# Optimization experiments

Hardware: AMD Instinct MI355X
Metric: run time of the kernel (lower is better)

The kernel has to match this reference:

```python
import jax, jax.numpy as jnp
import numpy as np

B, H, N, DK, DV = 2, 8, 2048, 64, 64

def setup_inputs() -> dict:
    key = jax.random.key(0)
    k1, k2, k3, k4 = jax.random.split(key, 4)
    q = jax.random.normal(k1, (B, H, N, DK), dtype=jnp.float32)
    k = jax.random.normal(k2, (B, H, N, DK), dtype=jnp.float32)
    v = jax.random.normal(k3, (B, H, N, DV), dtype=jnp.float32)
    # decay mask, strictly positive in (0,1)
    omask = jax.random.uniform(k4, (B, H, N, N), dtype=jnp.float32, minval=1e-3, maxval=1.0)
    return {"q": q, "k": k, "v": v, "omask": omask}

def reference(q, k, v, omask):
    # coefficients from the decay mask
    q_bar_coef = omask[..., :, 0] / jnp.sqrt(omask.sum(axis=-1))  # (B,H,n)
    k_bar_coef = 1.0 / omask[..., :, 0]                            # (B,H,n)
    q_bar = q_bar_coef[..., None] * q                               # (B,H,n,dk)
    k_bar = k_bar_coef[..., None] * k                               # (B,H,n,dk)
    # normalizer P (detached in original)
    T = jnp.cumsum(k_bar, axis=-2)                                  # (B,H,n,dk)
    P = jnp.einsum('bhia,bhia->bhi', T, q_bar)                      # (B,H,n)
    P = jnp.maximum(jnp.abs(jax.lax.stop_gradient(P)), 1.0)[..., None]
    # cumulative outer-product state D: (B,H,n,dk,dv)
    D = jnp.cumsum(jnp.einsum('bhia,bhic->bhiac', k_bar, v), axis=-3)
    O = jnp.einsum('bhia,bhiac->bhic', q_bar, D) / P                # (B,H,n,dv)
    return O
```

## Files before the change

kernel.cpp:

```cpp
#include <hip/hip_runtime.h>
#include <cmath>

constexpr int B_ = 2, H_ = 8, N_ = 2048, DK_ = 64, DV_ = 64;
constexpr int BH_ = B_ * H_;
constexpr int C_ = 64;
constexpr int NC_ = N_ / C_;
constexpr int NCH_ = BH_ * NC_;

__global__ __launch_bounds__(256) void coef_kernel(const float* __restrict__ om,
                                                   float* __restrict__ qc,
                                                   float* __restrict__ kc) {
  int row = blockIdx.x * 4 + (threadIdx.x >> 6);
  int lane = threadIdx.x & 63;
  const float* r = om + (size_t)row * N_;
  float s = 0.f;
#pragma unroll
  for (int kk = 0; kk < N_ / 256; ++kk) {
    float4 v4 = *(const float4*)(r + kk * 256 + lane * 4);
    s += (v4.x + v4.y) + (v4.z + v4.w);
  }
#pragma unroll
  for (int off = 32; off > 0; off >>= 1) s += __shfl_xor(s, off, 64);
  if (lane == 0) {
    float o0 = r[0];
    qc[row] = o0 / sqrtf(s);
    kc[row] = 1.0f / o0;
  }
}

__global__ __launch_bounds__(256) void chunksum_kernel(const float* __restrict__ kg,
                                                       const float* __restrict__ vg,
                                                       const float* __restrict__ kc,
                                                       float* __restrict__ ksum,
                                                       float* __restrict__ kvsum) {
  __shared__ float kb[C_][DK_];
  __shared__ float vs[C_][DV_];
  int chunk = blockIdx.x;
  int bh = chunk / NC_, ci = chunk - bh * NC_;
  int r0 = ci * C_;
  size_t gbase = ((size_t)bh * N_ + r0) * DK_;
  int t = threadIdx.x;
#pragma unroll
  for (int p = 0; p < 4; ++p) {
    int f = t + p * 256;
    int row = f >> 4, col = (f & 15) * 4;
    float sc = kc[bh * N_ + r0 + row];
    float4 k4 = *(const float4*)(kg + gbase + (size_t)f * 4);
    k4.x *= sc; k4.y *= sc; k4.z *= sc; k4.w *= sc;
    *(float4*)&kb[row][col] = k4;
    *(float4*)&vs[row][col] = *(const float4*)(vg + gbase + (size_t)f * 4);
  }
  __syncthreads();
  int dk0 = (t & 15) * 4, dv0 = (t >> 4) * 4;
  float acc[4][4] = {};
  float ks[4] = {};
  for (int r = 0; r < C_; ++r) {
    float4 k4 = *(const float4*)&kb[r][dk0];
    float4 v4 = *(const float4*)&vs[r][dv0];
    float ka[4] = {k4.x, k4.y, k4.z, k4.w};
    float va[4] = {v4.x, v4.y, v4.z, v4.w};
#pragma unroll
    for (int i = 0; i < 4; ++i) {
      ks[i] += ka[i];
#pragma unroll
      for (int j = 0; j < 4; ++j) acc[i][j] += ka[i] * va[j];
    }
  }
  float* kvc = kvsum + (size_t)chunk * (DK_ * DV_);
#pragma unroll
  for (int i = 0; i < 4; ++i) {
    float4 w = make_float4(acc[i][0], acc[i][1], acc[i][2], acc[i][3]);
    *(float4*)(kvc + (size_t)(dk0 + i) * DV_ + dv0) = w;
  }
  if (t < 16) {
#pragma unroll
    for (int i = 0; i < 4; ++i) ksum[(size_t)chunk * DK_ + dk0 + i] = ks[i];
  }
}

__global__ __launch_bounds__(256) void scan_kernel(float* __restrict__ ksum,
                                                   float* __restrict__ kvsum) {
  constexpr int PER = DK_ * DV_ + DK_;
  int idx = blockIdx.x * 256 + threadIdx.x;
  if (idx >= BH_ * PER) return;
  int bh = idx / PER, e = idx - bh * PER;
  float run = 0.f;
  if (e < DK_ * DV_) {
    float* p = kvsum + (size_t)bh * NC_ * (DK_ * DV_) + e;
    for (int ci = 0; ci < NC_; ++ci) {
      float tv = p[(size_t)ci * (DK_ * DV_)];
      p[(size_t)ci * (DK_ * DV_)] = run;
      run += tv;
    }
  } else {
    float* p = ksum + (size_t)bh * NC_ * DK_ + (e - DK_ * DV_);
    for (int ci = 0; ci < NC_; ++ci) {
      float tv = p[(size_t)ci * DK_];
      p[(size_t)ci * DK_] = run;
      run += tv;
    }
  }
}

__global__ __launch_bounds__(256) void out_kernel(const float* __restrict__ qg,
                                                  const float* __restrict__ kg,
                                                  const float* __restrict__ vg,
                                                  const float* __restrict__ qc,
                                                  const float* __restrict__ kc,
                                                  const float* __restrict__ ksum,
                                                  const float* __restrict__ kvsum,
                                                  float* __restrict__ outg) {
  __shared__ float qbT[DK_][C_];
  __shared__ float kbT[DK_][C_];
  __shared__ float vs[C_][DV_];
  int chunk = blockIdx.x;
  int bh = chunk / NC_, ci = chunk - bh * NC_;
  int r0 = ci * C_;
  size_t gbase = ((size_t)bh * N_ + r0) * DK_;
  int t = threadIdx.x;
  {
    int i = t & 63;
    int apart = t >> 6;
    float qsc = qc[bh * N_ + r0 + i];
    float ksc = kc[bh * N_ + r0 + i];
#pragma unroll
    for (int u = 0; u < 4; ++u) {
      int a0 = apart * 16 + u * 4;
      float4 q4 = *(const float4*)(qg + gbase + (size_t)i * DK_ + a0);
      float4 k4 = *(const float4*)(kg + gbase + (size_t)i * DK_ + a0);
      qbT[a0 + 0][i] = q4.x * qsc; qbT[a0 + 1][i] = q4.y * qsc;
      qbT[a0 + 2][i] = q4.z * qsc; qbT[a0 + 3][i] = q4.w * qsc;
      kbT[a0 + 0][i] = k4.x * ksc; kbT[a0 + 1][i] = k4.y * ksc;
      kbT[a0 + 2][i] = k4.z * ksc; kbT[a0 + 3][i] = k4.w * ksc;
    }
#pragma unroll
    for (int p = 0; p < 4; ++p) {
      int f = t + p * 256;
      int row = f >> 4, col = (f & 15) * 4;
      *(float4*)&vs[row][col] = *(const float4*)(vg + gbase + (size_t)f * 4);
    }
  }
  __syncthreads();

  int i0 = (t & 15) * 4, j0 = (t >> 4) * 4;
  float acc[4][4] = {};
  for (int a = 0; a < DK_; ++a) {
    float4 q4 = *(const float4*)&qbT[a][i0];
    float4 k4 = *(const float4*)&kbT[a][j0];
    float qa[4] = {q4.x, q4.y, q4.z, q4.w};
    float kk[4] = {k4.x, k4.y, k4.z, k4.w};
#pragma unroll
    for (int ii = 0; ii < 4; ++ii)
#pragma unroll
      for (int jj = 0; jj < 4; ++jj) acc[ii][jj] += qa[ii] * kk[jj];
  }
  __syncthreads();
  float (*St)[C_] = kbT;
#pragma unroll
  for (int jj = 0; jj < 4; ++jj) {
    int j = j0 + jj;
    float4 w;
    w.x = (j <= i0 + 0) ? acc[0][jj] : 0.f;
    w.y = (j <= i0 + 1) ? acc[1][jj] : 0.f;
    w.z = (j <= i0 + 2) ? acc[2][jj] : 0.f;
    w.w = (j <= i0 + 3) ? acc[3][jj] : 0.f;
    *(float4*)&St[j][i0] = w;
  }
  __syncthreads();

  {
    int bi0 = (t >> 4) * 4, c0 = (t & 15) * 4;
    const float* kvp = kvsum + (size_t)chunk * (DK_ * DV_);
    const float* tp = ksum + (size_t)chunk * DK_;
    float o[4][4] = {};
    float pp[4] = {};
    for (int a = 0; a < DK_; ++a) {
      float4 q4 = *(const float4*)&qbT[a][bi0];
      float4 d4 = *(const float4*)(kvp + (size_t)a * DV_ + c0);
      float tv = tp[a];
      float qa[4] = {q4.x, q4.y, q4.z, q4.w};
      float da[4] = {d4.x, d4.y, d4.z, d4.w};
#pragma unroll
      for (int ii = 0; ii < 4; ++ii) {
        pp[ii] += qa[ii] * tv;
#pragma unroll
        for (int cc = 0; cc < 4; ++cc) o[ii][cc] += qa[ii] * da[cc];
      }
    }
    for (int j = 0; j < C_; ++j) {
      float4 s4 = *(const float4*)&St[j][bi0];
      float4 v4 = *(const float4*)&vs[j][c0];
      float sa[4] = {s4.x, s4.y, s4.z, s4.w};
      float va[4] = {v4.x, v4.y, v4.z, v4.w};
#pragma unroll
      for (int ii = 0; ii < 4; ++ii) {
        pp[ii] += sa[ii];
#pragma unroll
        for (int cc = 0; cc < 4; ++cc) o[ii][cc] += sa[ii] * va[cc];
      }
    }
    float* ob = outg + ((size_t)bh * N_ + r0) * DV_;
#pragma unroll
    for (int ii = 0; ii < 4; ++ii) {
      float P = fmaxf(fabsf(pp[ii]), 1.0f);
      float inv = 1.0f / P;
      float4 w = make_float4(o[ii][0] * inv, o[ii][1] * inv,
                             o[ii][2] * inv, o[ii][3] * inv);
      *(float4*)(ob + (size_t)(bi0 + ii) * DV_ + c0) = w;
    }
  }
}

extern "C" void kernel_launch(void* const* d_in, const int* in_sizes, int n_in,
                              void* d_out, int out_size, void* d_ws, size_t ws_size,
                              hipStream_t stream) {
  const float* q = (const float*)d_in[0];
  const float* k = (const float*)d_in[1];
  const float* v = (const float*)d_in[2];
  const float* om = (const float*)d_in[3];
  float* out = (float*)d_out;

  float* ws = (float*)d_ws;
  float* qc = ws;
  float* kc = qc + BH_ * N_;
  float* ksum = kc + BH_ * N_;
  float* kv = ksum + (size_t)NCH_ * DK_;

  coef_kernel<<<BH_ * N_ / 4, 256, 0, stream>>>(om, qc, kc);
  chunksum_kernel<<<NCH_, 256, 0, stream>>>(k, v, kc, ksum, kv);
  constexpr int SCAN_TOTAL = BH_ * (DK_ * DV_ + DK_);
  scan_kernel<<<(SCAN_TOTAL + 255) / 256, 256, 0, stream>>>(ksum, kv);
  out_kernel<<<NCH_, 256, 0, stream>>>(q, k, v, qc, kc, ksum, kv, out);
}
```

Before: 77.06 us.

## Fuse coefficient, chunk-sum, scan and output into one cooperative kernel

Replaces the four-kernel pipeline with a single cooperative kernel of 512 blocks that uses grid-wide syncs between the chunk-sum, scan and output phases. Each block computes the omask row-sum coefficients for its own 64 rows, keeps q/k/v in registers across the phases, and writes the scan to separate buffers so it no longer works in place. This removes three kernel launches and the round trips of the coefficient arrays through global memory. In exchange it adds two grid barriers, needs all 512 blocks resident at once (launch_bounds 256,2), and runs the scan on only a fraction of the threads while the other blocks wait.

Result: slower. 193.0 us (+150.5%).

```diff
diff --git a/kernel.cpp b/kernel.cpp
--- a/kernel.cpp
+++ b/kernel.cpp
@@ -1,5 +1,8 @@
 #include <hip/hip_runtime.h>
+#include <hip/hip_cooperative_groups.h>
 #include <cmath>
+
+namespace cg = cooperative_groups;
 
 constexpr int B_ = 2, H_ = 8, N_ = 2048, DK_ = 64, DV_ = 64;
 constexpr int BH_ = B_ * H_;
@@ -7,138 +10,138 @@
 constexpr int NC_ = N_ / C_;
 constexpr int NCH_ = BH_ * NC_;
 
-__global__ __launch_bounds__(256) void coef_kernel(const float* __restrict__ om,
-                                                   float* __restrict__ qc,
-                                                   float* __restrict__ kc) {
-  int row = blockIdx.x * 4 + (threadIdx.x >> 6);
-  int lane = threadIdx.x & 63;
-  const float* r = om + (size_t)row * N_;
-  float s = 0.f;
-#pragma unroll
-  for (int kk = 0; kk < N_ / 256; ++kk) {
-    float4 v4 = *(const float4*)(r + kk * 256 + lane * 4);
-    s += (v4.x + v4.y) + (v4.z + v4.w);
-  }
-#pragma unroll
-  for (int off = 32; off > 0; off >>= 1) s += __shfl_xor(s, off, 64);
-  if (lane == 0) {
-    float o0 = r[0];
-    qc[row] = o0 / sqrtf(s);
-    kc[row] = 1.0f / o0;
-  }
-}
-
-__global__ __launch_bounds__(256) void chunksum_kernel(const float* __restrict__ kg,
-                                                       const float* __restrict__ vg,
-                                                       const float* __restrict__ kc,
-                                                       float* __restrict__ ksum,
-                                                       float* __restrict__ kvsum) {
+__global__ __launch_bounds__(256, 2) void fused_kernel(
+    const float* __restrict__ qg, const float* __restrict__ kg,
+    const float* __restrict__ vg, const float* __restrict__ om,
+    float* __restrict__ lksum, float* __restrict__ lkv,
+    float* __restrict__ pksum, float* __restrict__ pkv,
+    float* __restrict__ outg)
+{
   __shared__ float kb[C_][DK_];
+  __shared__ float kbT[DK_][C_];
   __shared__ float vs[C_][DV_];
-  int chunk = blockIdx.x;
-  int bh = chunk / NC_, ci = chunk - bh * NC_;
-  int r0 = ci * C_;
-  size_t gbase = ((size_t)bh * N_ + r0) * DK_;
-  int t = threadIdx.x;
+  __shared__ float smqc[C_], smkc[C_];
+
+  const int chunk = blockIdx.x;
+  const int bh = chunk >> 5, ci = chunk & 31;
+  const int r0 = ci * C_;
+  const size_t gbase = (size_t)(bh * N_ + r0) * DK_;
+  const int t = threadIdx.x;
+
+  float4 kr[4], vr[4], qr[4];
+#pragma unroll
+  for (int p = 0; p < 4; ++p) {
+    int f = t + p * 256;
+    kr[p] = *(const float4*)(kg + gbase + (size_t)f * 4);
+    vr[p] = *(const float4*)(vg + gbase + (size_t)f * 4);
+    qr[p] = *(const float4*)(qg + gbase + (size_t)f * 4);
+  }
+
+  {
+    const int w = t >> 6, lane = t & 63;
+    const float* ob = om + (size_t)(bh * N_ + r0) * N_;
+    for (int rr = 0; rr < 16; ++rr) {
+      const int row = w * 16 + rr;
+      const float* rp = ob + (size_t)row * N_;
+      float s = 0.f;
+#pragma unroll
+      for (int kk = 0; kk < 8; ++kk) {
+        float4 x = *(const float4*)(rp + kk * 256 + lane * 4);
+        s += (x.x + x.y) + (x.z + x.w);
+      }
+#pragma unroll
+      for (int off = 32; off; off >>= 1) s += __shfl_xor(s, off, 64);
+      if (lane == 0) {
+        float o0 = rp[0];
+        smqc[row] = o0 / sqrtf(s);
+        smkc[row] = 1.0f / o0;
+      }
+    }
+  }
+  __syncthreads();
+
 #pragma unroll
   for (int p = 0; p < 4; ++p) {
     int f = t + p * 256;
     int row = f >> 4, col = (f & 15) * 4;
-    float sc = kc[bh * N_ + r0 + row];
-    float4 k4 = *(const float4*)(kg + gbase + (size_t)f * 4);
+    float sc = smkc[row];
+    float4 k4 = kr[p];
     k4.x *= sc; k4.y *= sc; k4.z *= sc; k4.w *= sc;
     *(float4*)&kb[row][col] = k4;
-    *(float4*)&vs[row][col] = *(const float4*)(vg + gbase + (size_t)f * 4);
-  }
-  __syncthreads();
-  int dk0 = (t & 15) * 4, dv0 = (t >> 4) * 4;
-  float acc[4][4] = {};
-  float ks[4] = {};
-  for (int r = 0; r < C_; ++r) {
-    float4 k4 = *(const float4*)&kb[r][dk0];
-    float4 v4 = *(const float4*)&vs[r][dv0];
-    float ka[4] = {k4.x, k4.y, k4.z, k4.w};
-    float va[4] = {v4.x, v4.y, v4.z, v4.w};
-#pragma unroll
-    for (int i = 0; i < 4; ++i) {
-      ks[i] += ka[i];
-#pragma unroll
-      for (int j = 0; j < 4; ++j) acc[i][j] += ka[i] * va[j];
-    }
-  }
-  float* kvc = kvsum + (size_t)chunk * (DK_ * DV_);
-#pragma unroll
-  for (int i = 0; i < 4; ++i) {
-    float4 w = make_float4(acc[i][0], acc[i][1], acc[i][2], acc[i][3]);
-    *(float4*)(kvc + (size_t)(dk0 + i) * DV_ + dv0) = w;
-  }
-  if (t < 16) {
-#pragma unroll
-    for (int i = 0; i < 4; ++i) ksum[(size_t)chunk * DK_ + dk0 + i] = ks[i];
-  }
-}
-
-__global__ __launch_bounds__(256) void scan_kernel(float* __restrict__ ksum,
-                                                   float* __restrict__ kvsum) {
-  constexpr int PER = DK_ * DV_ + DK_;
-  int idx = blockIdx.x * 256 + threadIdx.x;
-  if (idx >= BH_ * PER) return;
-  int bh = idx / PER, e = idx - bh * PER;
-  float run = 0.f;
-  if (e < DK_ * DV_) {
-    float* p = kvsum + (size_t)bh * NC_ * (DK_ * DV_) + e;
-    for (int ci = 0; ci < NC_; ++ci) {
-      float tv = p[(size_t)ci * (DK_ * DV_)];
-      p[(size_t)ci * (DK_ * DV_)] = run;
-      run += tv;
-    }
-  } else {
-    float* p = ksum + (size_t)bh * NC_ * DK_ + (e - DK_ * DV_);
-    for (int ci = 0; ci < NC_; ++ci) {
-      float tv = p[(size_t)ci * DK_];
-      p[(size_t)ci * DK_] = run;
-      run += tv;
-    }
-  }
-}
-
-__global__ __launch_bounds__(256) void out_kernel(const float* __restrict__ qg,
-                                                  const float* __restrict__ kg,
-                                                  const float* __restrict__ vg,
-                                                  const float* __restrict__ qc,
-                                                  const float* __restrict__ kc,
-                                                  const float* __restrict__ ksum,
-                                                  const float* __restrict__ kvsum,
-                                                  float* __restrict__ outg) {
-  __shared__ float qbT[DK_][C_];
-  __shared__ float kbT[DK_][C_];
-  __shared__ float vs[C_][DV_];
-  int chunk = blockIdx.x;
-  int bh = chunk / NC_, ci = chunk - bh * NC_;
-  int r0 = ci * C_;
-  size_t gbase = ((size_t)bh * N_ + r0) * DK_;
-  int t = threadIdx.x;
-  {
-    int i = t & 63;
-    int apart = t >> 6;
-    float qsc = qc[bh * N_ + r0 + i];
-    float ksc = kc[bh * N_ + r0 + i];
-#pragma unroll
-    for (int u = 0; u < 4; ++u) {
-      int a0 = apart * 16 + u * 4;
-      float4 q4 = *(const float4*)(qg + gbase + (size_t)i * DK_ + a0);
-      float4 k4 = *(const float4*)(kg + gbase + (size_t)i * DK_ + a0);
-      qbT[a0 + 0][i] = q4.x * qsc; qbT[a0 + 1][i] = q4.y * qsc;
-      qbT[a0 + 2][i] = q4.z * qsc; qbT[a0 + 3][i] = q4.w * qsc;
-      kbT[a0 + 0][i] = k4.x * ksc; kbT[a0 + 1][i] = k4.y * ksc;
-      kbT[a0 + 2][i] = k4.z * ksc; kbT[a0 + 3][i] = k4.w * ksc;
-    }
-#pragma unroll
-    for (int p = 0; p < 4; ++p) {
-      int f = t + p * 256;
-      int row = f >> 4, col = (f & 15) * 4;
-      *(float4*)&vs[row][col] = *(const float4*)(vg + gbase + (size_t)f * 4);
-    }
+    kbT[col + 0][row] = k4.x;
+    kbT[col + 1][row] = k4.y;
+    kbT[col + 2][row] = k4.z;
+    kbT[col + 3][row] = k4.w;
+    *(float4*)&vs[row][col] = vr[p];
+  }
+  __syncthreads();
+  {
+    int dk0 = (t & 15) * 4, dv0 = (t >> 4) * 4;
+    float acc[4][4] = {};
+    float ks[4] = {};
+    for (int r = 0; r < C_; ++r) {
+      float4 k4 = *(const float4*)&kb[r][dk0];
+      float4 v4 = *(const float4*)&vs[r][dv0];
+      float ka[4] = {k4.x, k4.y, k4.z, k4.w};
+      float va[4] = {v4.x, v4.y, v4.z, v4.w};
+#pragma unroll
+      for (int i = 0; i < 4; ++i) {
+        ks[i] += ka[i];
+#pragma unroll
+        for (int j = 0; j < 4; ++j) acc[i][j] += ka[i] * va[j];
+      }
+    }
+    float* kvc = lkv + (size_t)chunk * (DK_ * DV_);
+#pragma unroll
+    for (int i = 0; i < 4; ++i)
+      *(float4*)(kvc + (size_t)(dk0 + i) * DV_ + dv0) =
+          make_float4(acc[i][0], acc[i][1], acc[i][2], acc[i][3]);
+    if (t < 16) {
+#pragma unroll
+      for (int i = 0; i < 4; ++i) lksum[(size_t)chunk * DK_ + dk0 + i] = ks[i];
+    }
+  }
+
+  cg::this_grid().sync();
+
+  {
+    constexpr int PER = DK_ * DV_ + DK_;
+    int g = blockIdx.x * 256 + t;
+    if (g < BH_ * PER) {
+      int sbh = g / PER, e = g - sbh * PER;
+      float run = 0.f;
+      if (e < DK_ * DV_) {
+        const float* src = lkv + (size_t)sbh * NC_ * (DK_ * DV_) + e;
+        float* dst = pkv + (size_t)sbh * NC_ * (DK_ * DV_) + e;
+        for (int cc = 0; cc < NC_; ++cc) {
+          dst[(size_t)cc * (DK_ * DV_)] = run;
+          run += src[(size_t)cc * (DK_ * DV_)];
+        }
+      } else {
+        int e2 = e - DK_ * DV_;
+        const float* src = lksum + (size_t)sbh * NC_ * DK_ + e2;
+        float* dst = pksum + (size_t)sbh * NC_ * DK_ + e2;
+        for (int cc = 0; cc < NC_; ++cc) {
+          dst[(size_t)cc * DK_] = run;
+          run += src[(size_t)cc * DK_];
+        }
+      }
+    }
+  }
+
+  cg::this_grid().sync();
+
+  float (*qbT)[C_] = (float(*)[C_])kb;
+#pragma unroll
+  for (int p = 0; p < 4; ++p) {
+    int f = t + p * 256;
+    int row = f >> 4, col = (f & 15) * 4;
+    float sc = smqc[row];
+    float4 q4 = qr[p];
+    qbT[col + 0][row] = q4.x * sc;
+    qbT[col + 1][row] = q4.y * sc;
+    qbT[col + 2][row] = q4.z * sc;
+    qbT[col + 3][row] = q4.w * sc;
   }
   __syncthreads();
 
@@ -170,8 +173,8 @@
 
   {
     int bi0 = (t >> 4) * 4, c0 = (t & 15) * 4;
-    const float* kvp = kvsum + (size_t)chunk * (DK_ * DV_);
-    const float* tp = ksum + (size_t)chunk * DK_;
+    const float* kvp = pkv + (size_t)chunk * (DK_ * DV_);
+    const float* tp = pksum + (size_t)chunk * DK_;
     float o[4][4] = {};
     float pp[4] = {};
     for (int a = 0; a < DK_; ++a) {
@@ -199,14 +202,14 @@
         for (int cc = 0; cc < 4; ++cc) o[ii][cc] += sa[ii] * va[cc];
       }
     }
-    float* ob = outg + ((size_t)bh * N_ + r0) * DV_;
+    float* obp = outg + (size_t)(bh * N_ + r0) * DV_;
 #pragma unroll
     for (int ii = 0; ii < 4; ++ii) {
       float P = fmaxf(fabsf(pp[ii]), 1.0f);
       float inv = 1.0f / P;
-      float4 w = make_float4(o[ii][0] * inv, o[ii][1] * inv,
-                             o[ii][2] * inv, o[ii][3] * inv);
-      *(float4*)(ob + (size_t)(bi0 + ii) * DV_ + c0) = w;
+      *(float4*)(obp + (size_t)(bi0 + ii) * DV_ + c0) =
+          make_float4(o[ii][0] * inv, o[ii][1] * inv,
+                      o[ii][2] * inv, o[ii][3] * inv);
     }
   }
 }
@@ -221,14 +224,14 @@
   float* out = (float*)d_out;
 
   float* ws = (float*)d_ws;
-  float* qc = ws;
-  float* kc = qc + BH_ * N_;
-  float* ksum = kc + BH_ * N_;
-  float* kv = ksum + (size_t)NCH_ * DK_;
-
-  coef_kernel<<<BH_ * N_ / 4, 256, 0, stream>>>(om, qc, kc);
-  chunksum_kernel<<<NCH_, 256, 0, stream>>>(k, v, kc, ksum, kv);
-  constexpr int SCAN_TOTAL = BH_ * (DK_ * DV_ + DK_);
-  scan_kernel<<<(SCAN_TOTAL + 255) / 256, 256, 0, stream>>>(ksum, kv);
-  out_kernel<<<NCH_, 256, 0, stream>>>(q, k, v, qc, kc, ksum, kv, out);
+  float* lksum = ws;
+  float* lkv = lksum + (size_t)NCH_ * DK_;
+  float* pksum = lkv + (size_t)NCH_ * DK_ * DV_;
+  float* pkv = pksum + (size_t)NCH_ * DK_;
+
+  void* args[] = {(void*)&q, (void*)&k, (void*)&v, (void*)&om,
+                  (void*)&lksum, (void*)&lkv, (void*)&pksum, (void*)&pkv,
+                  (void*)&out};
+  hipLaunchCooperativeKernel((void*)fused_kernel, dim3(NCH_), dim3(256),
+                             args, 0, stream);
 }
```

## Fuse coef, chunk sums, scan and output into one cooperative kernel

Applied to the files above, without the earlier changes.

Replaces the four-kernel pipeline with a single cooperative-launch kernel of 512 blocks × 1024 threads. Each block computes its chunk's coefficients from the mask, its local KV sums, a distributed scan after a grid sync, and the output after a second grid sync. The intra-chunk QK product and the inter-chunk Q·D product run concurrently in different thread groups. This removes three launch boundaries and the global round-trips for the coefficients, at the cost of two grid-wide barriers, 1024-thread blocks where many threads sit idle, and higher LDS use per block. If the cooperative launch fails, it falls back to the old kernels.

New measurement: 223.5 us. 190% more time.

```diff
diff --git a/kernel.cpp b/kernel.cpp
--- a/kernel.cpp
+++ b/kernel.cpp
@@ -1,11 +1,221 @@
 #include <hip/hip_runtime.h>
+#include <hip/hip_cooperative_groups.h>
 #include <cmath>
+
+namespace cg = cooperative_groups;
 
 constexpr int B_ = 2, H_ = 8, N_ = 2048, DK_ = 64, DV_ = 64;
 constexpr int BH_ = B_ * H_;
 constexpr int C_ = 64;
 constexpr int NC_ = N_ / C_;
 constexpr int NCH_ = BH_ * NC_;
+
+__global__ __launch_bounds__(1024, 8) void fused2(
+    const float* __restrict__ qg, const float* __restrict__ kg,
+    const float* __restrict__ vg, const float* __restrict__ om,
+    float* __restrict__ lksum, float* __restrict__ lkv,
+    float* __restrict__ pksum, float* __restrict__ pkv,
+    float* __restrict__ outg)
+{
+  __shared__ float kb[C_][DK_];
+  __shared__ float kbT[DK_][C_];
+  __shared__ float vs[C_][DV_];
+  __shared__ float qbT[DK_][C_];
+  __shared__ float smqc[C_], smkc[C_], ppm[C_];
+
+  const int chunk = blockIdx.x;
+  const int bh = chunk >> 5, ci = chunk & 31;
+  const int r0 = ci * C_;
+  const size_t gbase = (size_t)(bh * N_ + r0) * DK_;
+  const int t = threadIdx.x;
+
+  const float4 k4g = *(const float4*)(kg + gbase + (size_t)t * 4);
+  const float4 v4g = *(const float4*)(vg + gbase + (size_t)t * 4);
+  const float4 q4g = *(const float4*)(qg + gbase + (size_t)t * 4);
+
+  {
+    const int w = t >> 6, lane = t & 63;
+    const float* ob = om + (size_t)(bh * N_ + r0) * N_;
+    for (int rr = 0; rr < 4; ++rr) {
+      const int row = w * 4 + rr;
+      const float* rp = ob + (size_t)row * N_;
+      float s = 0.f;
+#pragma unroll
+      for (int kk = 0; kk < 8; ++kk) {
+        float4 x = *(const float4*)(rp + kk * 256 + lane * 4);
+        s += (x.x + x.y) + (x.z + x.w);
+      }
+#pragma unroll
+      for (int off = 32; off; off >>= 1) s += __shfl_xor(s, off, 64);
+      if (lane == 0) {
+        float o0 = rp[0];
+        smqc[row] = o0 / sqrtf(s);
+        smkc[row] = 1.0f / o0;
+      }
+    }
+  }
+  __syncthreads();
+
+  {
+    int row = t >> 4, col = (t & 15) * 4;
+    float kcv = smkc[row], qcv = smqc[row];
+    float4 k4 = k4g;
+    k4.x *= kcv; k4.y *= kcv; k4.z *= kcv; k4.w *= kcv;
+    *(float4*)&kb[row][col] = k4;
+    kbT[col + 0][row] = k4.x; kbT[col + 1][row] = k4.y;
+    kbT[col + 2][row] = k4.z; kbT[col + 3][row] = k4.w;
+    *(float4*)&vs[row][col] = v4g;
+    qbT[col + 0][row] = q4g.x * qcv; qbT[col + 1][row] = q4g.y * qcv;
+    qbT[col + 2][row] = q4g.z * qcv; qbT[col + 3][row] = q4g.w * qcv;
+  }
+  __syncthreads();
+
+  if (t < 256) {
+    int dk0 = (t & 15) * 4, dv0 = (t >> 4) * 4;
+    float acc[4][4] = {};
+    float ks[4] = {};
+    for (int r = 0; r < C_; ++r) {
+      float4 k4 = *(const float4*)&kb[r][dk0];
+      float4 v4 = *(const float4*)&vs[r][dv0];
+      float ka[4] = {k4.x, k4.y, k4.z, k4.w};
+      float va[4] = {v4.x, v4.y, v4.z, v4.w};
+#pragma unroll
+      for (int i = 0; i < 4; ++i) {
+        ks[i] += ka[i];
+#pragma unroll
+        for (int j = 0; j < 4; ++j) acc[i][j] += ka[i] * va[j];
+      }
+    }
+    float* kvc = lkv + (size_t)chunk * (DK_ * DV_);
+#pragma unroll
+    for (int i = 0; i < 4; ++i)
+      *(float4*)(kvc + (size_t)(dk0 + i) * DV_ + dv0) =
+          make_float4(acc[i][0], acc[i][1], acc[i][2], acc[i][3]);
+    if (t < 16) {
+#pragma unroll
+      for (int i = 0; i < 4; ++i) lksum[(size_t)chunk * DK_ + dk0 + i] = ks[i];
+    }
+  }
+
+  cg::this_grid().sync();
+
+  {
+    constexpr int PER = DK_ * DV_ + DK_;
+    int g = blockIdx.x * 130 + t;
+    if (t < 130) {
+      int sbh = g / PER, e = g - sbh * PER;
+      float run = 0.f;
+      if (e < DK_ * DV_) {
+        const float* src = lkv + (size_t)sbh * NC_ * (DK_ * DV_) + e;
+        float* dst = pkv + (size_t)sbh * NC_ * (DK_ * DV_) + e;
+        for (int cc = 0; cc < NC_; ++cc) {
+          dst[(size_t)cc * (DK_ * DV_)] = run;
+          run += src[(size_t)cc * (DK_ * DV_)];
+        }
+      } else {
+        int e2 = e - DK_ * DV_;
+        const float* src = lksum + (size_t)sbh * NC_ * DK_ + e2;
+        float* dst = pksum + (size_t)sbh * NC_ * DK_ + e2;
+        for (int cc = 0; cc < NC_; ++cc) {
+          dst[(size_t)cc * DK_] = run;
+          run += src[(size_t)cc * DK_];
+        }
+      }
+    }
+  }
+
+  cg::this_grid().sync();
+
+  float (*odm)[DK_] = kb;
+  float accS[4][4] = {};
+  if (t < 256) {
+    int i0 = (t & 15) * 4, j0 = (t >> 4) * 4;
+    for (int a = 0; a < DK_; ++a) {
+      float4 q4 = *(const float4*)&qbT[a][i0];
+      float4 k4 = *(const float4*)&kbT[a][j0];
+      float qa[4] = {q4.x, q4.y, q4.z, q4.w};
+      float kk[4] = {k4.x, k4.y, k4.z, k4.w};
+#pragma unroll
+      for (int ii = 0; ii < 4; ++ii)
+#pragma unroll
+        for (int jj = 0; jj < 4; ++jj) accS[ii][jj] += qa[ii] * kk[jj];
+    }
+  } else if (t < 512) {
+    int u = t - 256;
+    int bi0 = (u >> 4) * 4, c0 = (u & 15) * 4;
+    const float* kvp = pkv + (size_t)chunk * (DK_ * DV_);
+    const float* tp = pksum + (size_t)chunk * DK_;
+    float o1[4][4] = {};
+    float pp1[4] = {};
+    for (int a = 0; a < DK_; ++a) {
+      float4 q4 = *(const float4*)&qbT[a][bi0];
+      float4 d4 = *(const float4*)(kvp + (size_t)a * DV_ + c0);
+      float tv = tp[a];
+      float qa[4] = {q4.x, q4.y, q4.z, q4.w};
+      float da[4] = {d4.x, d4.y, d4.z, d4.w};
+#pragma unroll
+      for (int ii = 0; ii < 4; ++ii) {
+        pp1[ii] += qa[ii] * tv;
+#pragma unroll
+        for (int cc = 0; cc < 4; ++cc) o1[ii][cc] += qa[ii] * da[cc];
+      }
+    }
+#pragma unroll
+    for (int ii = 0; ii < 4; ++ii)
+      *(float4*)&odm[bi0 + ii][c0] =
+          make_float4(o1[ii][0], o1[ii][1], o1[ii][2], o1[ii][3]);
+    if ((u & 15) == 0) {
+#pragma unroll
+      for (int ii = 0; ii < 4; ++ii) ppm[bi0 + ii] = pp1[ii];
+    }
+  }
+  __syncthreads();
+  if (t < 256) {
+    int i0 = (t & 15) * 4, j0 = (t >> 4) * 4;
+    float (*St)[C_] = kbT;
+#pragma unroll
+    for (int jj = 0; jj < 4; ++jj) {
+      int j = j0 + jj;
+      float4 w;
+      w.x = (j <= i0 + 0) ? accS[0][jj] : 0.f;
+      w.y = (j <= i0 + 1) ? accS[1][jj] : 0.f;
+      w.z = (j <= i0 + 2) ? accS[2][jj] : 0.f;
+      w.w = (j <= i0 + 3) ? accS[3][jj] : 0.f;
+      *(float4*)&St[j][i0] = w;
+    }
+  }
+  __syncthreads();
+  if (t < 256) {
+    int bi0 = (t >> 4) * 4, c0 = (t & 15) * 4;
+    float (*St)[C_] = kbT;
+    float o[4][4] = {};
+    float ppS[4] = {};
+    for (int j = 0; j < C_; ++j) {
+      float4 s4 = *(const float4*)&St[j][bi0];
+      float4 v4 = *(const float4*)&vs[j][c0];
+      float sa[4] = {s4.x, s4.y, s4.z, s4.w};
+      float va[4] = {v4.x, v4.y, v4.z, v4.w};
+#pragma unroll
+      for (int ii = 0; ii < 4; ++ii) {
+        ppS[ii] += sa[ii];
+#pragma unroll
+        for (int cc = 0; cc < 4; ++cc) o[ii][cc] += sa[ii] * va[cc];
+      }
+    }
+    float* obp = outg + (size_t)(bh * N_ + r0) * DV_;
+#pragma unroll
+    for (int ii = 0; ii < 4; ++ii) {
+      int row = bi0 + ii;
+      float P = fmaxf(fabsf(ppm[row] + ppS[ii]), 1.0f);
+      float inv = 1.0f / P;
+      float4 w = make_float4((o[ii][0] + odm[row][c0 + 0]) * inv,
+                             (o[ii][1] + odm[row][c0 + 1]) * inv,
+                             (o[ii][2] + odm[row][c0 + 2]) * inv,
+                             (o[ii][3] + odm[row][c0 + 3]) * inv);
+      *(float4*)(obp + (size_t)row * DV_ + c0) = w;
+    }
+  }
+}
 
 __global__ __launch_bounds__(256) void coef_kernel(const float* __restrict__ om,
                                                    float* __restrict__ qc,
@@ -68,36 +278,37 @@
   }
   float* kvc = kvsum + (size_t)chunk * (DK_ * DV_);
 #pragma unroll
-  for (int i = 0; i < 4; ++i) {
-    float4 w = make_float4(acc[i][0], acc[i][1], acc[i][2], acc[i][3]);
-    *(float4*)(kvc + (size_t)(dk0 + i) * DV_ + dv0) = w;
-  }
+  for (int i = 0; i < 4; ++i)
+    *(float4*)(kvc + (size_t)(dk0 + i) * DV_ + dv0) =
+        make_float4(acc[i][0], acc[i][1], acc[i][2], acc[i][3]);
   if (t < 16) {
 #pragma unroll
     for (int i = 0; i < 4; ++i) ksum[(size_t)chunk * DK_ + dk0 + i] = ks[i];
   }
 }
 
-__global__ __launch_bounds__(256) void scan_kernel(float* __restrict__ ksum,
-                                                   float* __restrict__ kvsum) {
+__global__ __launch_bounds__(256) void scan_kernel(const float* __restrict__ lks,
+                                                   const float* __restrict__ lkv,
+                                                   float* __restrict__ pks,
+                                                   float* __restrict__ pkv) {
   constexpr int PER = DK_ * DV_ + DK_;
   int idx = blockIdx.x * 256 + threadIdx.x;
   if (idx >= BH_ * PER) return;
   int bh = idx / PER, e = idx - bh * PER;
   float run = 0.f;
   if (e < DK_ * DV_) {
-    float* p = kvsum + (size_t)bh * NC_ * (DK_ * DV_) + e;
+    const float* src = lkv + (size_t)bh * NC_ * (DK_ * DV_) + e;
+    float* dst = pkv + (size_t)bh * NC_ * (DK_ * DV_) + e;
     for (int ci = 0; ci < NC_; ++ci) {
-      float tv = p[(size_t)ci * (DK_ * DV_)];
-      p[(size_t)ci * (DK_ * DV_)] = run;
-      run += tv;
+      dst[(size_t)ci * (DK_ * DV_)] = run;
+      run += src[(size_t)ci * (DK_ * DV_)];
     }
   } else {
-    float* p = ksum + (size_t)bh * NC_ * DK_ + (e - DK_ * DV_);
+    const float* src = lks + (size_t)bh * NC_ * DK_ + (e - DK_ * DV_);
+    float* dst = pks + (size_t)bh * NC_ * DK_ + (e - DK_ * DV_);
     for (int ci = 0; ci < NC_; ++ci) {
-      float tv = p[(size_t)ci * DK_];
-      p[(size_t)ci * DK_] = run;
-      run += tv;
+      dst[(size_t)ci * DK_] = run;
+      run += src[(size_t)ci * DK_];
     }
   }
 }
@@ -141,7 +352,6 @@
     }
   }
   __syncthreads();
-
   int i0 = (t & 15) * 4, j0 = (t >> 4) * 4;
   float acc[4][4] = {};
   for (int a = 0; a < DK_; ++a) {
@@ -167,7 +377,6 @@
     *(float4*)&St[j][i0] = w;
   }
   __syncthreads();
-
   {
     int bi0 = (t >> 4) * 4, c0 = (t & 15) * 4;
     const float* kvp = kvsum + (size_t)chunk * (DK_ * DV_);
@@ -199,14 +408,14 @@
         for (int cc = 0; cc < 4; ++cc) o[ii][cc] += sa[ii] * va[cc];
       }
     }
-    float* ob = outg + ((size_t)bh * N_ + r0) * DV_;
+    float* obp = outg + ((size_t)bh * N_ + r0) * DV_;
 #pragma unroll
     for (int ii = 0; ii < 4; ++ii) {
       float P = fmaxf(fabsf(pp[ii]), 1.0f);
       float inv = 1.0f / P;
-      float4 w = make_float4(o[ii][0] * inv, o[ii][1] * inv,
-                             o[ii][2] * inv, o[ii][3] * inv);
-      *(float4*)(ob + (size_t)(bi0 + ii) * DV_ + c0) = w;
+      *(float4*)(obp + (size_t)(bi0 + ii) * DV_ + c0) =
+          make_float4(o[ii][0] * inv, o[ii][1] * inv,
+                      o[ii][2] * inv, o[ii][3] * inv);
     }
   }
 }
@@ -221,14 +430,24 @@
   float* out = (float*)d_out;
 
   float* ws = (float*)d_ws;
-  float* qc = ws;
-  float* kc = qc + BH_ * N_;
-  float* ksum = kc + BH_ * N_;
-  float* kv = ksum + (size_t)NCH_ * DK_;
-
-  coef_kernel<<<BH_ * N_ / 4, 256, 0, stream>>>(om, qc, kc);
-  chunksum_kernel<<<NCH_, 256, 0, stream>>>(k, v, kc, ksum, kv);
-  constexpr int SCAN_TOTAL = BH_ * (DK_ * DV_ + DK_);
-  scan_kernel<<<(SCAN_TOTAL + 255) / 256, 256, 0, stream>>>(ksum, kv);
-  out_kernel<<<NCH_, 256, 0, stream>>>(q, k, v, qc, kc, ksum, kv, out);
-}
+  float* lksum = ws;
+  float* lkv = lksum + (size_t)NCH_ * DK_;
+  float* pksum = lkv + (size_t)NCH_ * DK_ * DV_;
+  float* pkv = pksum + (size_t)NCH_ * DK_;
+
+  void* args[] = {(void*)&q, (void*)&k, (void*)&v, (void*)&om,
+                  (void*)&lksum, (void*)&lkv, (void*)&pksum, (void*)&pkv,
+                  (void*)&out};
+  hipError_t err = hipLaunchCooperativeKernel((void*)fused2, dim3(NCH_),
+                                              dim3(1024), args, 0, stream);
+  if (err != hipSuccess) {
+    float* qc = pkv + (size_t)NCH_ * DK_ * DV_;
+    float* kc = qc + BH_ * N_;
+    coef_kernel<<<BH_ * N_ / 4, 256, 0, stream>>>(om, qc, kc);
+    chunksum_kernel<<<NCH_, 256, 0, stream>>>(k, v, kc, lksum, lkv);
+    constexpr int SCAN_TOTAL = BH_ * (DK_ * DV_ + DK_);
+    scan_kernel<<<(SCAN_TOTAL + 255) / 256, 256, 0, stream>>>(lksum, lkv,
+                                                              pksum, pkv);
+    out_kernel<<<NCH_, 256, 0, stream>>>(q, k, v, qc, kc, pksum, pkv, out);
+  }
+}
```

## Rewrite output kernel with bf16 MFMA matmuls and fp32 prefix-scan normalizer

Applied to the files above, without the earlier changes.

Replaces the scalar FMA output kernel with one that converts q, k, v and the chunk state to bf16 in swizzled shared memory. It then uses 32x32x16 bf16 MFMA instructions for the intra-chunk QK^T and for the S·V + Q·D products. The normalizer P is now computed separately in fp32 through a shared-memory Hillis-Steele prefix scan over k_bar, then applied as a per-row reciprocal. The aim is to move the dominant dense work onto matrix cores. The cost is bf16 rounding error in the output plus extra scan barriers.

New measurement: 68.06 us, median of 2. 11.7% less time.

```diff
diff --git a/kernel.cpp b/kernel.cpp
--- a/kernel.cpp
+++ b/kernel.cpp
@@ -6,6 +6,20 @@
 constexpr int C_ = 64;
 constexpr int NC_ = N_ / C_;
 constexpr int NCH_ = BH_ * NC_;
+
+using f32x16 = __attribute__((ext_vector_type(16))) float;
+using bf16x8 = __attribute__((ext_vector_type(8))) __bf16;
+
+__device__ inline unsigned short bfr(float x) {
+  unsigned u = __float_as_uint(x);
+  return (unsigned short)((u + 0x7FFFu + ((u >> 16) & 1u)) >> 16);
+}
+__device__ inline unsigned pk2(float lo, float hi) {
+  return (unsigned)bfr(lo) | ((unsigned)bfr(hi) << 16);
+}
+__device__ inline int swi(int row, int a) {
+  return (row * 128 + (((a * 2) ^ ((row & 7) << 4)))) >> 1;
+}
 
 __global__ __launch_bounds__(256) void coef_kernel(const float* __restrict__ om,
                                                    float* __restrict__ qc,
@@ -68,10 +82,9 @@
   }
   float* kvc = kvsum + (size_t)chunk * (DK_ * DV_);
 #pragma unroll
-  for (int i = 0; i < 4; ++i) {
-    float4 w = make_float4(acc[i][0], acc[i][1], acc[i][2], acc[i][3]);
-    *(float4*)(kvc + (size_t)(dk0 + i) * DV_ + dv0) = w;
-  }
+  for (int i = 0; i < 4; ++i)
+    *(float4*)(kvc + (size_t)(dk0 + i) * DV_ + dv0) =
+        make_float4(acc[i][0], acc[i][1], acc[i][2], acc[i][3]);
   if (t < 16) {
 #pragma unroll
     for (int i = 0; i < 4; ++i) ksum[(size_t)chunk * DK_ + dk0 + i] = ks[i];
@@ -102,112 +115,155 @@
   }
 }
 
-__global__ __launch_bounds__(256) void out_kernel(const float* __restrict__ qg,
-                                                  const float* __restrict__ kg,
-                                                  const float* __restrict__ vg,
-                                                  const float* __restrict__ qc,
-                                                  const float* __restrict__ kc,
-                                                  const float* __restrict__ ksum,
-                                                  const float* __restrict__ kvsum,
-                                                  float* __restrict__ outg) {
-  __shared__ float qbT[DK_][C_];
-  __shared__ float kbT[DK_][C_];
-  __shared__ float vs[C_][DV_];
-  int chunk = blockIdx.x;
-  int bh = chunk / NC_, ci = chunk - bh * NC_;
-  int r0 = ci * C_;
-  size_t gbase = ((size_t)bh * N_ + r0) * DK_;
-  int t = threadIdx.x;
+__global__ __launch_bounds__(256) void out_mfma_kernel(
+    const float* __restrict__ qg, const float* __restrict__ kg,
+    const float* __restrict__ vg, const float* __restrict__ qc,
+    const float* __restrict__ kc, const float* __restrict__ ksum,
+    const float* __restrict__ kvsum, float* __restrict__ outg) {
+  __shared__ unsigned short qb[64 * 64];
+  __shared__ unsigned short kb[64 * 64];
+  __shared__ unsigned short sS[64 * 64];
+  __shared__ unsigned short vT[64 * 64];
+  __shared__ unsigned short dT[64 * 64];
+  __shared__ float Tc[2][64][68];
+  __shared__ float Tl[64];
+  __shared__ float Pf[64];
+
+  const int chunk = blockIdx.x;
+  const int bh = chunk >> 5, ci = chunk & 31;
+  const int r0 = ci * C_;
+  const int rowb = bh * N_ + r0;
+  const size_t gbase = (size_t)rowb * DK_;
+  const int t = threadIdx.x;
+  const int i = t >> 2, a0 = (t & 3) * 16;
+
+  float xq[16];
   {
-    int i = t & 63;
-    int apart = t >> 6;
-    float qsc = qc[bh * N_ + r0 + i];
-    float ksc = kc[bh * N_ + r0 + i];
-#pragma unroll
-    for (int u = 0; u < 4; ++u) {
-      int a0 = apart * 16 + u * 4;
-      float4 q4 = *(const float4*)(qg + gbase + (size_t)i * DK_ + a0);
-      float4 k4 = *(const float4*)(kg + gbase + (size_t)i * DK_ + a0);
-      qbT[a0 + 0][i] = q4.x * qsc; qbT[a0 + 1][i] = q4.y * qsc;
-      qbT[a0 + 2][i] = q4.z * qsc; qbT[a0 + 3][i] = q4.w * qsc;
-      kbT[a0 + 0][i] = k4.x * ksc; kbT[a0 + 1][i] = k4.y * ksc;
-      kbT[a0 + 2][i] = k4.z * ksc; kbT[a0 + 3][i] = k4.w * ksc;
-    }
-#pragma unroll
-    for (int p = 0; p < 4; ++p) {
-      int f = t + p * 256;
-      int row = f >> 4, col = (f & 15) * 4;
-      *(float4*)&vs[row][col] = *(const float4*)(vg + gbase + (size_t)f * 4);
-    }
+    float qcv = qc[rowb + i];
+    float kcv = kc[rowb + i];
+    float xk[16], xv[16], xd[16];
+    {
+      const float* qp = qg + gbase + (size_t)i * 64 + a0;
+      const float* kp = kg + gbase + (size_t)i * 64 + a0;
+      const float* vp = vg + gbase + (size_t)i * 64 + a0;
+      const float* dp = kvsum + (size_t)chunk * (DK_ * DV_) + (size_t)i * 64 + a0;
+#pragma unroll
+      for (int u = 0; u < 4; ++u) {
+        *(float4*)&xq[u * 4] = *(const float4*)(qp + u * 4);
+        *(float4*)&xk[u * 4] = *(const float4*)(kp + u * 4);
+        *(float4*)&xv[u * 4] = *(const float4*)(vp + u * 4);
+        *(float4*)&xd[u * 4] = *(const float4*)(dp + u * 4);
+      }
+    }
+#pragma unroll
+    for (int u = 0; u < 16; ++u) { xq[u] *= qcv; xk[u] *= kcv; }
+#pragma unroll
+    for (int u4 = 0; u4 < 4; ++u4)
+      *(float4*)&Tc[0][i][a0 + u4 * 4] = *(const float4*)&xk[u4 * 4];
+    unsigned* qbu = (unsigned*)qb;
+    unsigned* kbu = (unsigned*)kb;
+#pragma unroll
+    for (int u = 0; u < 8; ++u) {
+      int a = a0 + 2 * u;
+      int bi = (i * 128 + (((a * 2) ^ ((i & 7) << 4)))) >> 2;
+      qbu[bi] = pk2(xq[2 * u], xq[2 * u + 1]);
+      kbu[bi] = pk2(xk[2 * u], xk[2 * u + 1]);
+    }
+#pragma unroll
+    for (int u = 0; u < 16; ++u) {
+      int c = a0 + u;
+      vT[swi(c, i)] = bfr(xv[u]);
+      dT[swi(c, i)] = bfr(xd[u]);
+    }
+    if (t < 64) Tl[t] = ksum[(size_t)chunk * DK_ + t];
   }
   __syncthreads();
 
-  int i0 = (t & 15) * 4, j0 = (t >> 4) * 4;
-  float acc[4][4] = {};
-  for (int a = 0; a < DK_; ++a) {
-    float4 q4 = *(const float4*)&qbT[a][i0];
-    float4 k4 = *(const float4*)&kbT[a][j0];
-    float qa[4] = {q4.x, q4.y, q4.z, q4.w};
-    float kk[4] = {k4.x, k4.y, k4.z, k4.w};
-#pragma unroll
-    for (int ii = 0; ii < 4; ++ii)
-#pragma unroll
-      for (int jj = 0; jj < 4; ++jj) acc[ii][jj] += qa[ii] * kk[jj];
+  {
+    int p = 0;
+#pragma unroll
+    for (int step = 1; step < 64; step <<= 1) {
+      float4 cur[4], prv[4];
+#pragma unroll
+      for (int u4 = 0; u4 < 4; ++u4) {
+        cur[u4] = *(const float4*)&Tc[p][i][a0 + u4 * 4];
+        if (i >= step)
+          prv[u4] = *(const float4*)&Tc[p][i - step][a0 + u4 * 4];
+        else
+          prv[u4] = make_float4(0.f, 0.f, 0.f, 0.f);
+      }
+#pragma unroll
+      for (int u4 = 0; u4 < 4; ++u4) {
+        float4 w = make_float4(cur[u4].x + prv[u4].x, cur[u4].y + prv[u4].y,
+                               cur[u4].z + prv[u4].z, cur[u4].w + prv[u4].w);
+        *(float4*)&Tc[p ^ 1][i][a0 + u4 * 4] = w;
+      }
+      __syncthreads();
+      p ^= 1;
+    }
+  }
+
+  {
+    float part = 0.f;
+#pragma unroll
+    for (int u = 0; u < 16; ++u)
+      part += xq[u] * (Tl[a0 + u] + Tc[0][i][a0 + u]);
+    part += __shfl_xor(part, 1, 64);
+    part += __shfl_xor(part, 2, 64);
+    if ((t & 3) == 0) Pf[i] = 1.0f / fmaxf(fabsf(part), 1.0f);
+  }
+
+  const int lane = t & 63, w = t >> 6;
+  const int wr = w >> 1, wc = w & 1;
+  const int half = lane >> 5, col = lane & 31;
+  const int arow = 32 * wr + col;
+  const int bcol = 32 * wc + col;
+
+  f32x16 accS;
+#pragma unroll
+  for (int r = 0; r < 16; ++r) accS[r] = 0.f;
+#pragma unroll
+  for (int kk = 0; kk < 4; ++kk) {
+    int aa = kk * 16 + half * 8;
+    bf16x8 af = *(const bf16x8*)&qb[swi(arow, aa)];
+    bf16x8 bf = *(const bf16x8*)&kb[swi(bcol, aa)];
+    accS = __builtin_amdgcn_mfma_f32_32x32x16_bf16(af, bf, accS, 0, 0, 0);
+  }
+#pragma unroll
+  for (int r = 0; r < 16; ++r) {
+    int iloc = (r & 3) + 8 * (r >> 2) + 4 * half;
+    int ii = 32 * wr + iloc;
+    int jj = 32 * wc + col;
+    float m = (jj <= ii) ? accS[r] : 0.f;
+    sS[swi(ii, jj)] = bfr(m);
   }
   __syncthreads();
-  float (*St)[C_] = kbT;
-#pragma unroll
-  for (int jj = 0; jj < 4; ++jj) {
-    int j = j0 + jj;
-    float4 w;
-    w.x = (j <= i0 + 0) ? acc[0][jj] : 0.f;
-    w.y = (j <= i0 + 1) ? acc[1][jj] : 0.f;
-    w.z = (j <= i0 + 2) ? acc[2][jj] : 0.f;
-    w.w = (j <= i0 + 3) ? acc[3][jj] : 0.f;
-    *(float4*)&St[j][i0] = w;
-  }
-  __syncthreads();
-
-  {
-    int bi0 = (t >> 4) * 4, c0 = (t & 15) * 4;
-    const float* kvp = kvsum + (size_t)chunk * (DK_ * DV_);
-    const float* tp = ksum + (size_t)chunk * DK_;
-    float o[4][4] = {};
-    float pp[4] = {};
-    for (int a = 0; a < DK_; ++a) {
-      float4 q4 = *(const float4*)&qbT[a][bi0];
-      float4 d4 = *(const float4*)(kvp + (size_t)a * DV_ + c0);
-      float tv = tp[a];
-      float qa[4] = {q4.x, q4.y, q4.z, q4.w};
-      float da[4] = {d4.x, d4.y, d4.z, d4.w};
-#pragma unroll
-      for (int ii = 0; ii < 4; ++ii) {
-        pp[ii] += qa[ii] * tv;
-#pragma unroll
-        for (int cc = 0; cc < 4; ++cc) o[ii][cc] += qa[ii] * da[cc];
-      }
-    }
-    for (int j = 0; j < C_; ++j) {
-      float4 s4 = *(const float4*)&St[j][bi0];
-      float4 v4 = *(const float4*)&vs[j][c0];
-      float sa[4] = {s4.x, s4.y, s4.z, s4.w};
-      float va[4] = {v4.x, v4.y, v4.z, v4.w};
-#pragma unroll
-      for (int ii = 0; ii < 4; ++ii) {
-        pp[ii] += sa[ii];
-#pragma unroll
-        for (int cc = 0; cc < 4; ++cc) o[ii][cc] += sa[ii] * va[cc];
-      }
-    }
-    float* ob = outg + ((size_t)bh * N_ + r0) * DV_;
-#pragma unroll
-    for (int ii = 0; ii < 4; ++ii) {
-      float P = fmaxf(fabsf(pp[ii]), 1.0f);
-      float inv = 1.0f / P;
-      float4 w = make_float4(o[ii][0] * inv, o[ii][1] * inv,
-                             o[ii][2] * inv, o[ii][3] * inv);
-      *(float4*)(ob + (size_t)(bi0 + ii) * DV_ + c0) = w;
-    }
+
+  f32x16 acc;
+#pragma unroll
+  for (int r = 0; r < 16; ++r) acc[r] = 0.f;
+#pragma unroll
+  for (int kk = 0; kk < 4; ++kk) {
+    int j0 = kk * 16 + half * 8;
+    bf16x8 af = *(const bf16x8*)&sS[swi(arow, j0)];
+    bf16x8 bf = *(const bf16x8*)&vT[swi(bcol, j0)];
+    acc = __builtin_amdgcn_mfma_f32_32x32x16_bf16(af, bf, acc, 0, 0, 0);
+  }
+#pragma unroll
+  for (int kk = 0; kk < 4; ++kk) {
+    int aa = kk * 16 + half * 8;
+    bf16x8 af = *(const bf16x8*)&qb[swi(arow, aa)];
+    bf16x8 bf = *(const bf16x8*)&dT[swi(bcol, aa)];
+    acc = __builtin_amdgcn_mfma_f32_32x32x16_bf16(af, bf, acc, 0, 0, 0);
+  }
+
+  float* ob = outg + (size_t)rowb * DV_;
+#pragma unroll
+  for (int r = 0; r < 16; ++r) {
+    int iloc = (r & 3) + 8 * (r >> 2) + 4 * half;
+    int ii = 32 * wr + iloc;
+    int cc = 32 * wc + col;
+    ob[(size_t)ii * DV_ + cc] = acc[r] * Pf[ii];
   }
 }
 
@@ -230,5 +286,5 @@
   chunksum_kernel<<<NCH_, 256, 0, stream>>>(k, v, kc, ksum, kv);
   constexpr int SCAN_TOTAL = BH_ * (DK_ * DV_ + DK_);
   scan_kernel<<<(SCAN_TOTAL + 255) / 256, 256, 0, stream>>>(ksum, kv);
-  out_kernel<<<NCH_, 256, 0, stream>>>(q, k, v, qc, kc, ksum, kv, out);
-}
+  out_mfma_kernel<<<NCH_, 256, 0, stream>>>(q, k, v, qc, kc, ksum, kv, out);
+}
```
